# Kernel optimization log

Hardware: AMD Instinct MI355X
Metric: run time of the kernel (lower is better)

## Reference

```python
import jax, jax.numpy as jnp
import numpy as np

T = 1048576      # signal length
K = 3            # number of IMFs
ALPHA = 2000.0   # bandwidth penalty
TAU = 1e-7       # dual ascent step
TOL = 1e-6       # convergence tolerance
N_ITER = 50      # max fixed-point iterations


def _vmd(x, omega_init):
    T_ = x.shape[0]
    t = jnp.arange(1, T_ + 1, dtype=jnp.float32) / T_
    freqs = t - 0.5 - 1.0 / T_                           # [T]
    f_hat = jnp.fft.fftshift(jnp.fft.fft(x))             # [T] complex
    u0 = jnp.zeros((K, T_), dtype=f_hat.dtype)
    lam0 = jnp.zeros((T_,), dtype=f_hat.dtype)

    def step(carry, n):
        u_prev, lam_prev, omega, done = carry
        base = (freqs[None, :] - omega[:, None]) ** 2    # [K,T]
        # mode k's denom also gets (freqs-omega[k-1])^2 and (freqs-omega[k+1])^2
        nbr = jnp.zeros_like(base).at[1:].add(base[:-1]).at[:-1].add(base[1:])
        denom = base + nbr + TAU ** 2
        u_hat = (f_hat[None, :] - lam_prev[None, :] / 2.0) / (1.0 + ALPHA * denom)
        pw = jnp.real(u_hat) ** 2 + jnp.imag(u_hat) ** 2  # |u_hat|^2, [K,T]
        omega_new = jnp.sum(freqs[None, :] * pw, axis=1) / jnp.sum(pw, axis=1)
        lam_new = lam_prev + TAU * (jnp.sum(u_hat, axis=0) - f_hat)
        # convergence check (every 10th iter), mirrors the original break
        u_diff = jnp.sum(jnp.abs(u_hat - u_prev) ** 2) / jnp.sum(jnp.abs(u_prev) ** 2)
        om_diff = jnp.sum(jnp.abs(omega_new - jnp.roll(omega_new, 1))) / K
        conv = (n % 10 == 0) & (u_diff < TOL) & (om_diff < TOL)
        # freeze state once converged (break-iteration's fresh u_hat is kept)
        u_out = jnp.where(done, u_prev, u_hat)
        lam_out = jnp.where(done, lam_prev, lam_new)
        om_out = jnp.where(done, omega, omega_new)
        return (u_out, lam_out, om_out, done | conv), None

    init = (u0, lam0, omega_init.astype(jnp.float32), jnp.array(False))
    (u_hat, _, _, _), _ = jax.lax.scan(jax.checkpoint(step), init, jnp.arange(N_ITER))
    imfs = jnp.real(jnp.fft.ifft(jnp.fft.ifftshift(u_hat, axes=-1), axis=-1))
    return imfs.astype(jnp.float32)                      # [K,T]


def setup_inputs() -> dict:
    key = jax.random.key(0)
    kx, ko = jax.random.split(key)
    x = jax.random.normal(kx, (T,), dtype=jnp.float32)
    omega_init = jax.random.uniform(ko, (K,), dtype=jnp.float32) * 0.5  # init==1
    return {"x": x, "omega_init": omega_init}


def reference(x, omega_init):
    return _vmd(x, omega_init)
```

## Files before the change

kernel.cpp:

```cpp
#include <hip/hip_runtime.h>
#include <math.h>


#define ALPHA_F 2000.0f

static __device__ __forceinline__ int lpad2(int i) { return i + (i >> 4); }
static __device__ __forceinline__ int swz(int i)  { return ((i & 7) << 7) | (i >> 3); }
static __device__ __forceinline__ int swzA(int i) { return ((i & 7) << 6) | (i >> 3); }
static __device__ __forceinline__ float frcp(float x) { return __builtin_amdgcn_rcpf(x); }

typedef float v2f __attribute__((ext_vector_type(2)));
static __device__ __forceinline__ v2f sp(float s) { v2f r; r.x = s; r.y = s; return r; }
static __device__ __forceinline__ v2f v2(float a, float b) { v2f r; r.x = a; r.y = b; return r; }
static __device__ __forceinline__ v2f pkfma(v2f a, v2f b, v2f c)
{ return __builtin_elementwise_fma(a, b, c); }
static __device__ __forceinline__ v2f cmul(v2f a, v2f w)
{
  v2f t = a * sp(w.x);
  v2f s = v2(-a.y, a.x);
  return pkfma(s, sp(w.y), t);
}
static __device__ __forceinline__ v2f cmulrr(v2f a, float wr, float wi)
{
  v2f t = a * sp(wr);
  v2f s = v2(-a.y, a.x);
  return pkfma(s, sp(wi), t);
}

#define PADN2 1088

template<int CTRL>
static __device__ __forceinline__ float dpp_addf(float v)
{
  int r = __builtin_amdgcn_update_dpp(0, __float_as_int(v), CTRL, 0xf, 0xf, true);
  return v + __int_as_float(r);
}
static __device__ __forceinline__ float wave64_sum(float v)
{
  v = dpp_addf<0x111>(v);
  v = dpp_addf<0x112>(v);
  v = dpp_addf<0x114>(v);
  v = dpp_addf<0x118>(v);
  v = dpp_addf<0x142>(v);
  v = dpp_addf<0x143>(v);
  return v;
}
static __device__ __forceinline__ float row4_sum(float v)
{
  v = dpp_addf<0x111>(v);
  v = dpp_addf<0x112>(v);
  return v;
}
static __device__ __forceinline__ float rdlane(float v, int l)
{
  return __int_as_float(__builtin_amdgcn_readlane(__float_as_int(v), l));
}

template<int SIGN>
static __device__ __forceinline__ void bfly4(v2f Y0, v2f Y1, v2f Y2, v2f Y3,
    float w1r, float w1i, float w2r, float w2i, float w3r, float w3i,
    v2f& o0, v2f& o1, v2f& o2, v2f& o3)
{
  v2f y1 = cmulrr(Y1, w1r, w1i), y2 = cmulrr(Y2, w2r, w2i),
      y3 = cmulrr(Y3, w3r, w3i);
  v2f t0 = Y0 + y2, t1 = Y0 - y2, t2 = y1 + y3, t3 = y1 - y3;
  o0 = t0 + t2; o2 = t0 - t2;
  v2f ns3 = v2(t3.y, -t3.x);
  if (SIGN < 0) { o1 = t1 + ns3; o3 = t1 - ns3; }
  else          { o1 = t1 - ns3; o3 = t1 + ns3; }
}
template<int SIGN>
static __device__ __forceinline__ void bfly4_nt(v2f X0, v2f X1, v2f X2, v2f X3,
    v2f& o0, v2f& o1, v2f& o2, v2f& o3)
{
  v2f t0 = X0 + X2, t1 = X0 - X2, t2 = X1 + X3, t3 = X1 - X3;
  o0 = t0 + t2; o2 = t0 - t2;
  v2f ns3 = v2(t3.y, -t3.x);
  if (SIGN < 0) { o1 = t1 + ns3; o3 = t1 - ns3; }
  else          { o1 = t1 - ns3; o3 = t1 + ns3; }
}

template<int SIGN>
static __device__ void fft1024p_reg(v2f X0, v2f X1, v2f X2, v2f X3,
                                    v2f* A, v2f* B)
{
  const int u = threadIdx.x;
  {
    v2f o0, o1, o2, o3;
    bfly4_nt<SIGN>(X0, X1, X2, X3, o0, o1, o2, o3);
    const int base = u << 2;
    B[lpad2(base    )] = o0; B[lpad2(base + 1)] = o1;
    B[lpad2(base + 2)] = o2; B[lpad2(base + 3)] = o3;
    __syncthreads();
  }
#pragma unroll
  for (int st = 1; st < 5; ++st) {
    v2f *in  = (st & 1) ? B : A;
    v2f *out = (st & 1) ? A : B;
    const int quarter = 1 << (2 * st);
    const int p = u & (quarter - 1);
    const int g = u >> (2 * st);

    float sw, cw;
    sincospif((float)(2 * p) * (1.0f / (float)(4 << (2 * st))), &sw, &cw);
    const float w1r = cw, w1i = (SIGN < 0) ? -sw : sw;
    const float w2r = w1r * w1r - w1i * w1i, w2i = 2.0f * w1r * w1i;
    const float w3r = w2r * w1r - w2i * w1i, w3i = w2r * w1i + w2i * w1r;

    v2f o0, o1, o2, o3;
    bfly4<SIGN>(in[lpad2(u)], in[lpad2(u + 256)],
                in[lpad2(u + 512)], in[lpad2(u + 768)],
                w1r, w1i, w2r, w2i, w3r, w3i, o0, o1, o2, o3);

    const int base = (g << (2 * st + 2)) + p;
    out[lpad2(base              )] = o0;
    out[lpad2(base +     quarter)] = o1;
    out[lpad2(base + 2 * quarter)] = o2;
    out[lpad2(base + 3 * quarter)] = o3;
    __syncthreads();
  }
}

__global__ __launch_bounds__(256) void k_fwd_passA(const float* __restrict__ x,
                                                   float2* __restrict__ ws0)
{
  __shared__ __align__(16) v2f A[PADN2], B[PADN2];
  const int p = swzA(blockIdx.x);
  const int tid = threadIdx.x;
  const int c0 = 2 * p;
  v2f X[4];
#pragma unroll
  for (int q = 0; q < 4; ++q)
    X[q] = ((const v2f*)x)[(size_t)(tid + 256 * q) * 512 + p];
  fft1024p_reg<-1>(X[0], X[1], X[2], X[3], A, B);

  float sa, ca, sb, cb, ssa, cca, ssb, ccb;
  sincospif((float)(c0 * tid) * (2.0f / 1048576.0f), &sa, &ca);
  sincospif((float)((c0 + 1) * tid) * (2.0f / 1048576.0f), &sb, &cb);
  sincospif((float)c0 * (1.0f / 2048.0f), &ssa, &cca);
  sincospif((float)(c0 + 1) * (1.0f / 2048.0f), &ssb, &ccb);
  v2f E0 = v2(ca, -sa), E1 = v2(cb, -sb);
  const v2f S0 = v2(cca, -ssa), S1 = v2(ccb, -ssb);
#pragma unroll
  for (int q = 0; q < 2; ++q) {
    int k = tid + 256 * q;
    int kk = (1024 - k) & 1023;
    v2f Z = B[lpad2(k)];
    v2f Wv = B[lpad2(kk)];
    float X0r = 0.5f * (Z.x + Wv.x), X0i = 0.5f * (Z.y - Wv.y);
    float X1r = 0.5f * (Z.y + Wv.y), X1i = 0.5f * (Wv.x - Z.x);
    v2f o01 = cmul(v2(X0r, X0i), E0);
    v2f o23 = cmul(v2(X1r, X1i), E1);
    float4 o = make_float4(o01.x, o01.y, o23.x, o23.y);
    ((float4*)ws0)[(size_t)k * 512 + p] = o;
    if (q == 0) { E0 = cmul(E0, S0); E1 = cmul(E1, S1); }
  }
  if (tid == 0) {
    v2f Z = B[lpad2(512)];
    float s0, c0f, s1, c1f;
    sincospif((float)c0 * (1.0f / 1024.0f), &s0, &c0f);
    sincospif((float)(c0 + 1) * (1.0f / 1024.0f), &s1, &c1f);
    v2f o01 = cmul(v2(Z.x, 0.0f), v2(c0f, -s0));
    v2f o23 = cmul(v2(Z.y, 0.0f), v2(c1f, -s1));
    float4 o = make_float4(o01.x, o01.y, o23.x, o23.y);
    ((float4*)ws0)[(size_t)512 * 512 + p] = o;
  }
}

__global__ __launch_bounds__(256) void k_fwd_passB(const float2* __restrict__ ws0,
                                                   float2* __restrict__ fhat,
                                                   float* __restrict__ ET)
{
  __shared__ __align__(16) v2f A[PADN2], B[PADN2];
  const int b = blockIdx.x;
  const int tid = threadIdx.x;
  v2f X[4];
#pragma unroll
  for (int q = 0; q < 4; ++q)
    X[q] = ((const v2f*)ws0)[(size_t)b * 1024 + tid + 256 * q];
  fft1024p_reg<-1>(X[0], X[1], X[2], X[3], A, B);
  const bool mir = (b >= 1) && (b <= 511);
#pragma unroll
  for (int q = 0; q < 4; ++q) {
    int k2 = tid + 256 * q;
    v2f v = B[lpad2(k2)];
    float e = v.x * v.x + v.y * v.y;
    fhat[(size_t)b * 1024 + k2] = make_float2(v.x, v.y);
    ET[(size_t)k2 * 1024 + b] = e;
    if (mir) {
      fhat[(size_t)(1024 - b) * 1024 + (1023 - k2)] = make_float2(v.x, -v.y);
      ET[(size_t)(1023 - k2) * 1024 + (1024 - b)] = e;
    }
  }
}

static __device__ __forceinline__ void lag4(float x, float& l0, float& l1,
                                            float& l2, float& l3)
{
  float m0 = x, m1 = x - (1.0f / 3.0f), m2 = x - (2.0f / 3.0f), m3 = x - 1.0f;
  l0 = -4.5f * m1 * m2 * m3;
  l1 = 13.5f * m0 * m2 * m3;
  l2 = -13.5f * m0 * m1 * m3;
  l3 =  4.5f * m0 * m1 * m2;
}

__global__ __launch_bounds__(256) void k_moments(const float* __restrict__ ET,
                                                 double* __restrict__ W)
{
  __shared__ double red[4 * 4];
  const int B = blockIdx.x;
  const int k2 = B ^ 512;
  const int tid = threadIdx.x;
  double a0 = 0, a1 = 0, a2 = 0, a3 = 0;
#pragma unroll
  for (int q = 0; q < 4; ++q) {
    int k1 = tid + 256 * q;
    float e = ET[(size_t)k2 * 1024 + k1];
    float l0, l1, l2, l3;
    lag4((float)k1 * (1.0f / 1024.0f), l0, l1, l2, l3);
    a0 += (double)(e * l0); a1 += (double)(e * l1);
    a2 += (double)(e * l2); a3 += (double)(e * l3);
  }
  const int lane = tid & 63, wv = tid >> 6;
  double pv[4] = { a0, a1, a2, a3 };
#pragma unroll
  for (int j = 0; j < 4; ++j) {
    double v = pv[j];
    for (int off = 32; off; off >>= 1) v += __shfl_down(v, off, 64);
    if (lane == 0) red[wv * 4 + j] = v;
  }
  __syncthreads();
  if (tid < 4)
    W[B * 4 + tid] = red[tid] + red[4 + tid] + red[8 + tid] + red[12 + tid];
}

__global__ __launch_bounds__(256) void k_solve(
    const double* __restrict__ W4, const float* __restrict__ omega_init,
    float* __restrict__ omegaF)
{
  __shared__ float red[2][64];
  const int t = threadIdx.x;
  const int lane = t & 63, wv = t >> 6;

  float Wsc[16], fsc[16];
#pragma unroll
  for (int e = 0; e < 16; ++e) {
    Wsc[e] = (float)W4[t * 16 + e];
    int bin = 4 * t + (e >> 2);
    fsc[e] = (float)((double)bin / 1024.0 + (double)(e & 3) / 3072.0 - 0.5);
  }
  v2f frA[8], WrA[8], WfA[8];
#pragma unroll
  for (int i = 0; i < 8; ++i) {
    frA[i] = v2(fsc[2 * i], fsc[2 * i + 1]);
    WrA[i] = v2(Wsc[2 * i], Wsc[2 * i + 1]);
    WfA[i] = WrA[i] * frA[i];
  }
  float om0 = omega_init[0], om1 = omega_init[1], om2 = omega_init[2];

#pragma unroll 1
  for (int it = 0; it < 49; ++it) {
    float* rb = red[it & 1];
    v2f p0 = sp(0.f), p1 = sp(0.f), p2 = sp(0.f),
        p3 = sp(0.f), p4 = sp(0.f), p5 = sp(0.f);

#pragma unroll
    for (int i = 0; i < 8; ++i) {
      const v2f fv = frA[i];
      v2f a0 = fv - sp(om0), a1 = fv - sp(om1), a2 = fv - sp(om2);
      v2f t0 = sp(ALPHA_F) * a0, t1 = sp(ALPHA_F) * a1, t2 = sp(ALPHA_F) * a2;
      v2f m1 = pkfma(t1, a1, sp(1.0f));
      v2f dA = pkfma(t0, a0, m1);
      v2f dC = pkfma(t2, a2, m1);
      v2f dB = pkfma(t2, a2, dA);
      v2f AB = dA * dB, BC = dB * dC, AC = dA * dC;
      v2f ABC = AB * dC;
      float rr = frcp(ABC.x * ABC.y);
      v2f r = v2(rr * ABC.y, rr * ABC.x);
      v2f v0 = r * BC, v1 = r * AC, v2_ = r * AB;
      v2f g0 = v0 * v0, g1 = v1 * v1, g2 = v2_ * v2_;
      p0 = pkfma(WfA[i], g0, p0); p1 = pkfma(WfA[i], g1, p1);
      p2 = pkfma(WfA[i], g2, p2);
      p3 = pkfma(WrA[i], g0, p3); p4 = pkfma(WrA[i], g1, p4);
      p5 = pkfma(WrA[i], g2, p5);
    }

    float q0 = p0.x + p0.y, q1 = p1.x + p1.y, q2 = p2.x + p2.y;
    float q3 = p3.x + p3.y, q4 = p4.x + p4.y, q5 = p5.x + p5.y;

    q0 = wave64_sum(q0); q1 = wave64_sum(q1); q2 = wave64_sum(q2);
    q3 = wave64_sum(q3); q4 = wave64_sum(q4); q5 = wave64_sum(q5);
    if (lane == 63) {
      rb[0 * 4 + wv] = q0; rb[1 * 4 + wv] = q1; rb[2 * 4 + wv] = q2;
      rb[3 * 4 + wv] = q3; rb[4 * 4 + wv] = q4; rb[5 * 4 + wv] = q5;
    }
    __syncthreads();
    float v1r = red[it & 1][lane];
    v1r = row4_sum(v1r);
    float n0 = rdlane(v1r, 3),  n1 = rdlane(v1r, 7),  n2 = rdlane(v1r, 11);
    float e0 = rdlane(v1r, 15), e1 = rdlane(v1r, 19), e2 = rdlane(v1r, 23);
    float ie01 = frcp(e0 * e1);
    om0 = n0 * (ie01 * e1);
    om1 = n1 * (ie01 * e0);
    om2 = n2 * frcp(e2);
  }

  if (t == 0) { omegaF[0] = om0; omegaF[1] = om1; omegaF[2] = om2; }
}

__global__ __launch_bounds__(256) void k_inv_A2(
    const float2* __restrict__ fhat, const float* __restrict__ omegaF,
    float2* __restrict__ ws0)
{
  __shared__ __align__(16) v2f A[PADN2], B[PADN2];
  const int tid = threadIdx.x;
  const int bb = blockIdx.x;
  const bool pl1 = (bb >= 1024);
  const int b = pl1 ? ((bb == 1536) ? 512 : swzA(bb - 1024)) : swz(bb);
  const float om0 = omegaF[0], om1 = omegaF[1], om2 = omegaF[2];

  v2f X[4];
#pragma unroll
  for (int q = 0; q < 4; ++q) {
    int j = tid + 256 * q;
    float2 f = fhat[(size_t)b * 1024 + j];
    int bin = j ^ 512;
    int tt = (bin << 10) | b;
    float freq = (float)tt * (1.0f / 1048576.0f) - 0.5f;
    v2f fpm = v2(freq, -freq);
    v2f A0 = fpm - sp(om0), A1v = fpm - sp(om1), A2v = fpm - sp(om2);
    v2f D0 = A0 * A0, D1 = A1v * A1v, D2 = A2v * A2v;
    if (!pl1) {
      v2f DA = pkfma(sp(ALPHA_F), D0 + D1, sp(1.0f));
      v2f DB = pkfma(sp(ALPHA_F), D2, DA);
      float rrA = frcp(DA.x * DA.y);
      float rrB = frcp(DB.x * DB.y);
      float Rr = 0.5f * (rrA * DA.y + rrA * DA.x);
      float Ri = 0.5f * (rrB * DB.y + rrB * DB.x);
      X[q] = cmul(v2(f.x, f.y), v2(Rr, Ri));
    } else {
      v2f DC = pkfma(sp(ALPHA_F), D1 + D2, sp(1.0f));
      float rrC = frcp(DC.x * DC.y);
      float Rr2 = 0.5f * (rrC * DC.y + rrC * DC.x);
      X[q] = v2(f.x, f.y) * sp(Rr2);
    }
  }
  fft1024p_reg<1>(X[0], X[1], X[2], X[3], A, B);

  float sa, ca, ss, cs;
  sincospif((float)(b * tid) * (2.0f / 1048576.0f), &sa, &ca);
  sincospif((float)b * (1.0f / 2048.0f), &ss, &cs);
  v2f E = v2(ca, sa);
  const v2f S = v2(cs, ss);

  if (!pl1) {
#pragma unroll
    for (int q = 0; q < 4; ++q) {
      int m1i = tid + 256 * q;
      v2f va = B[lpad2(m1i)];
      v2f oa = cmul(va, E);
      ws0[(size_t)m1i * 1024 + b] = make_float2(oa.x, oa.y);
      E = cmul(E, S);
    }
  } else {
    const bool mir = (b >= 1) && (b <= 511);
#pragma unroll
    for (int q = 0; q < 4; ++q) {
      int m1i = tid + 256 * q;
      v2f vb = B[lpad2(m1i)];
      v2f ob = cmul(vb, E);
      ws0[1048576 + (size_t)m1i * 1024 + b] = make_float2(ob.x, ob.y);
      if (mir)
        ws0[1048576 + (size_t)m1i * 1024 + (1024 - b)] = make_float2(ob.x, -ob.y);
      E = cmul(E, S);
    }
  }
}

__global__ __launch_bounds__(256) void k_inv_B2(const float2* __restrict__ ws0,
                                                float* __restrict__ out)
{
  __shared__ __align__(16) v2f A[PADN2], B[PADN2];
  const int tid = threadIdx.x;
  const float sc = 1.0f / 1048576.0f;

  if (blockIdx.x < 1024) {
    const int b = swz(blockIdx.x);
    v2f X[4];
#pragma unroll
    for (int q = 0; q < 4; ++q)
      X[q] = ((const v2f*)ws0)[(size_t)b * 1024 + tid + 256 * q];
    fft1024p_reg<1>(X[0], X[1], X[2], X[3], A, B);
#pragma unroll
    for (int q = 0; q < 4; ++q) {
      int m2 = tid + 256 * q;
      v2f v = B[lpad2(m2)];
      out[(size_t)m2 * 1024 + b]           = v.x * sc;
      out[1048576 + (size_t)m2 * 1024 + b] = v.y * sc;
    }
  } else {
    const int s = swzA(blockIdx.x - 1024);
    const int b0 = 2 * s, b1 = 2 * s + 1;
#pragma unroll
    for (int q = 0; q < 4; ++q) {
      int j = tid + 256 * q;
      A[lpad2(j)] = ((const v2f*)ws0)[1048576 + (size_t)b0 * 1024 + j];
      B[lpad2(j)] = ((const v2f*)ws0)[1048576 + (size_t)b1 * 1024 + j];
    }
    __syncthreads();
    v2f Z[4];
#pragma unroll
    for (int q = 0; q < 4; ++q) {
      int j = tid + 256 * q;
      int mj = (1024 - j) & 1023;
      v2f W0j = A[lpad2(j)], W0m = A[lpad2(mj)];
      v2f W1j = B[lpad2(j)], W1m = B[lpad2(mj)];
      float H0r = 0.5f * (W0j.x + W0m.x), H0i = 0.5f * (W0j.y - W0m.y);
      float H1r = 0.5f * (W1j.x + W1m.x), H1i = 0.5f * (W1j.y - W1m.y);
      Z[q] = v2(H0r - H1i, H0i + H1r);
    }
    __syncthreads();
    fft1024p_reg<1>(Z[0], Z[1], Z[2], Z[3], A, B);
#pragma unroll
    for (int q = 0; q < 4; ++q) {
      int m2 = tid + 256 * q;
      v2f v = B[lpad2(m2)];
      out[2097152 + (size_t)m2 * 1024 + b0] = v.x * sc;
      out[2097152 + (size_t)m2 * 1024 + b1] = v.y * sc;
    }
  }
}

extern "C" void kernel_launch(void* const* d_in, const int* in_sizes, int n_in,
                              void* d_out, int out_size, void* d_ws, size_t ws_size,
                              hipStream_t stream)
{
  (void)in_sizes; (void)n_in; (void)out_size; (void)ws_size;
  const float* x       = (const float*)d_in[0];
  const float* om_init = (const float*)d_in[1];
  float* out = (float*)d_out;

  char* w = (char*)d_ws;
  const size_t MB = 1024ull * 1024ull;
  float2* fhat     = (float2*)(w);
  float*  ET       = (float*)(w + 8 * MB);
  double* W4       = (double*)(w + 12 * MB);
  float*  omegaF   = (float*)(w + 12 * MB + 48 * 1024);
  float2* scratch  = (float2*)(w + 16 * MB);

  k_fwd_passA<<<512, 256, 0, stream>>>(x, scratch);
  k_fwd_passB<<<513, 256, 0, stream>>>(scratch, fhat, ET);
  k_moments<<<1024, 256, 0, stream>>>(ET, W4);
  k_solve<<<1, 256, 0, stream>>>(W4, om_init, omegaF);
  k_inv_A2<<<1537, 256, 0, stream>>>(fhat, omegaF, scratch);
  k_inv_B2<<<1536, 256, 0, stream>>>(scratch, out);
}
```

Before: 161.5 us.

## Replace inverse FFT reconstruction with truncated time-domain convolution kernels

Instead of storing the full spectrum and running a two-pass inverse FFT per mode, the code builds three short real symmetric impulse responses (128 lags) from the Wiener-style filters at the solved omegas. It then convolves x directly in the time domain. This removes the fhat writes and both inverse FFT kernels, trading them for a small kernel-build pass with atomics and a cheap shared-memory convolution. It relies on the Lorentzian filter's impulse response decaying fast enough for a 128-lag truncation to stay within tolerance.

```diff
diff --git a/kernel.cpp b/kernel.cpp
--- a/kernel.cpp
+++ b/kernel.cpp
@@ -3,9 +3,9 @@
 
 
 #define ALPHA_F 2000.0f
+#define LAGS 128
 
 static __device__ __forceinline__ int lpad2(int i) { return i + (i >> 4); }
-static __device__ __forceinline__ int swz(int i)  { return ((i & 7) << 7) | (i >> 3); }
 static __device__ __forceinline__ int swzA(int i) { return ((i & 7) << 6) | (i >> 3); }
 static __device__ __forceinline__ float frcp(float x) { return __builtin_amdgcn_rcpf(x); }
 
@@ -168,7 +168,6 @@
 }
 
 __global__ __launch_bounds__(256) void k_fwd_passB(const float2* __restrict__ ws0,
-                                                   float2* __restrict__ fhat,
                                                    float* __restrict__ ET)
 {
   __shared__ __align__(16) v2f A[PADN2], B[PADN2];
@@ -185,12 +184,9 @@
     int k2 = tid + 256 * q;
     v2f v = B[lpad2(k2)];
     float e = v.x * v.x + v.y * v.y;
-    fhat[(size_t)b * 1024 + k2] = make_float2(v.x, v.y);
     ET[(size_t)k2 * 1024 + b] = e;
-    if (mir) {
-      fhat[(size_t)(1024 - b) * 1024 + (1023 - k2)] = make_float2(v.x, -v.y);
+    if (mir)
       ET[(size_t)(1023 - k2) * 1024 + (1024 - b)] = e;
-    }
   }
 }
 
@@ -236,7 +232,7 @@
 
 __global__ __launch_bounds__(256) void k_solve(
     const double* __restrict__ W4, const float* __restrict__ omega_init,
-    float* __restrict__ omegaF)
+    float* __restrict__ omegaF, float* __restrict__ kerf)
 {
   __shared__ float red[2][64];
   const int t = threadIdx.x;
@@ -305,129 +301,111 @@
     om2 = n2 * frcp(e2);
   }
 
+  for (int i = t; i < 384; i += 256) kerf[i] = 0.0f;
   if (t == 0) { omegaF[0] = om0; omegaF[1] = om1; omegaF[2] = om2; }
 }
 
-__global__ __launch_bounds__(256) void k_inv_A2(
-    const float2* __restrict__ fhat, const float* __restrict__ omegaF,
-    float2* __restrict__ ws0)
-{
-  __shared__ __align__(16) v2f A[PADN2], B[PADN2];
+__global__ __launch_bounds__(256) void k_kerbuild(const float* __restrict__ omegaF,
+                                                  float* __restrict__ kerf)
+{
+  __shared__ __align__(16) float Rs[3][2048];
   const int tid = threadIdx.x;
-  const int bb = blockIdx.x;
-  const bool pl1 = (bb >= 1024);
-  const int b = pl1 ? ((bb == 1536) ? 512 : swzA(bb - 1024)) : swz(bb);
+  const int b = blockIdx.x;
   const float om0 = omegaF[0], om1 = omegaF[1], om2 = omegaF[2];
-
-  v2f X[4];
-#pragma unroll
-  for (int q = 0; q < 4; ++q) {
-    int j = tid + 256 * q;
-    float2 f = fhat[(size_t)b * 1024 + j];
-    int bin = j ^ 512;
-    int tt = (bin << 10) | b;
-    float freq = (float)tt * (1.0f / 1048576.0f) - 0.5f;
-    v2f fpm = v2(freq, -freq);
-    v2f A0 = fpm - sp(om0), A1v = fpm - sp(om1), A2v = fpm - sp(om2);
-    v2f D0 = A0 * A0, D1 = A1v * A1v, D2 = A2v * A2v;
-    if (!pl1) {
-      v2f DA = pkfma(sp(ALPHA_F), D0 + D1, sp(1.0f));
-      v2f DB = pkfma(sp(ALPHA_F), D2, DA);
-      float rrA = frcp(DA.x * DA.y);
-      float rrB = frcp(DB.x * DB.y);
-      float Rr = 0.5f * (rrA * DA.y + rrA * DA.x);
-      float Ri = 0.5f * (rrB * DB.y + rrB * DB.x);
-      X[q] = cmul(v2(f.x, f.y), v2(Rr, Ri));
-    } else {
-      v2f DC = pkfma(sp(ALPHA_F), D1 + D2, sp(1.0f));
-      float rrC = frcp(DC.x * DC.y);
-      float Rr2 = 0.5f * (rrC * DC.y + rrC * DC.x);
-      X[q] = v2(f.x, f.y) * sp(Rr2);
+  const int f0 = b * 2048;
+#pragma unroll
+  for (int q = 0; q < 8; ++q) {
+    int idx = q * 256 + tid;
+    int fi = f0 + idx;
+    float nu = (float)(fi - 524288) * (1.0f / 1048576.0f);
+    float a0 = nu - om0, a1 = nu - om1, a2 = nu - om2;
+    float d0 = a0 * a0, d1 = a1 * a1, d2 = a2 * a2;
+    float tA = fmaf(ALPHA_F, d0 + d1, 1.0f);
+    float tB = fmaf(ALPHA_F, d2, tA);
+    float tC = fmaf(ALPHA_F, d1 + d2, 1.0f);
+    Rs[0][idx] = frcp(tA);
+    Rs[1][idx] = frcp(tB);
+    Rs[2][idx] = frcp(tC);
+  }
+  __syncthreads();
+  const int s = tid;
+  if (s >= LAGS) return;
+  float ws_, wc_;
+  sincospif((float)(4 * s) * (1.0f / 1048576.0f), &ws_, &wc_);
+  v2f acc0 = sp(0.f), acc1 = sp(0.f), acc2 = sp(0.f);
+#pragma unroll 1
+  for (int quar = 0; quar < 4; ++quar) {
+    int ubase = quar * 512;
+    v2f cr, ci;
+    {
+      float cv[2], sv[2];
+#pragma unroll
+      for (int l = 0; l < 2; ++l) {
+        int fi = f0 + ubase + l;
+        int m = (2 * s * fi) & 2097151;
+        float arg = (float)m * (1.0f / 1048576.0f);
+        float sv_, cv_;
+        sincospif(arg, &sv_, &cv_);
+        if (s & 1) { sv_ = -sv_; cv_ = -cv_; }
+        cv[l] = cv_; sv[l] = sv_;
+      }
+      cr = v2(cv[0], cv[1]); ci = v2(sv[0], sv[1]);
     }
-  }
-  fft1024p_reg<1>(X[0], X[1], X[2], X[3], A, B);
-
-  float sa, ca, ss, cs;
-  sincospif((float)(b * tid) * (2.0f / 1048576.0f), &sa, &ca);
-  sincospif((float)b * (1.0f / 2048.0f), &ss, &cs);
-  v2f E = v2(ca, sa);
-  const v2f S = v2(cs, ss);
-
-  if (!pl1) {
-#pragma unroll
-    for (int q = 0; q < 4; ++q) {
-      int m1i = tid + 256 * q;
-      v2f va = B[lpad2(m1i)];
-      v2f oa = cmul(va, E);
-      ws0[(size_t)m1i * 1024 + b] = make_float2(oa.x, oa.y);
-      E = cmul(E, S);
+#pragma unroll 4
+    for (int it = 0; it < 256; ++it) {
+      int u = ubase + 2 * it;
+      v2f r0 = *(const v2f*)&Rs[0][u];
+      v2f r1 = *(const v2f*)&Rs[1][u];
+      v2f r2 = *(const v2f*)&Rs[2][u];
+      acc0 = pkfma(r0, cr, acc0);
+      acc1 = pkfma(r1, cr, acc1);
+      acc2 = pkfma(r2, cr, acc2);
+      v2f ncr = pkfma(ci, sp(-ws_), cr * sp(wc_));
+      v2f nci = pkfma(cr, sp(ws_), ci * sp(wc_));
+      cr = ncr; ci = nci;
     }
-  } else {
-    const bool mir = (b >= 1) && (b <= 511);
-#pragma unroll
-    for (int q = 0; q < 4; ++q) {
-      int m1i = tid + 256 * q;
-      v2f vb = B[lpad2(m1i)];
-      v2f ob = cmul(vb, E);
-      ws0[1048576 + (size_t)m1i * 1024 + b] = make_float2(ob.x, ob.y);
-      if (mir)
-        ws0[1048576 + (size_t)m1i * 1024 + (1024 - b)] = make_float2(ob.x, -ob.y);
-      E = cmul(E, S);
+  }
+  const float sc = 1.0f / 1048576.0f;
+  atomicAdd(&kerf[s],       (acc0.x + acc0.y) * sc);
+  atomicAdd(&kerf[128 + s], (acc1.x + acc1.y) * sc);
+  atomicAdd(&kerf[256 + s], (acc2.x + acc2.y) * sc);
+}
+
+__global__ __launch_bounds__(256) void k_conv(const float* __restrict__ x,
+                                              const float* __restrict__ kerf,
+                                              float* __restrict__ out)
+{
+  __shared__ float xs[766];
+  __shared__ __align__(8) float kp01[2 * LAGS];
+  __shared__ float kp2[LAGS];
+  const int tid = threadIdx.x;
+  const int B = blockIdx.x;
+  const int base = B * 512 - 127;
+  for (int i = tid; i < 766; i += 256)
+    xs[i] = x[(base + i) & 1048575];
+  if (tid < LAGS) {
+    kp01[2 * tid]     = kerf[tid];
+    kp01[2 * tid + 1] = kerf[128 + tid];
+    kp2[tid]          = kerf[256 + tid];
+  }
+  __syncthreads();
+#pragma unroll
+  for (int r = 0; r < 2; ++r) {
+    int tl = r * 256 + tid;
+    int off = 127 + tl;
+    float xc = xs[off];
+    v2f a01 = (*(const v2f*)&kp01[0]) * sp(xc);
+    float a2 = kp2[0] * xc;
+#pragma unroll 4
+    for (int s = 1; s < LAGS; ++s) {
+      float pa = xs[off - s] + xs[off + s];
+      a01 = pkfma(*(const v2f*)&kp01[2 * s], sp(pa), a01);
+      a2 = fmaf(kp2[s], pa, a2);
     }
-  }
-}
-
-__global__ __launch_bounds__(256) void k_inv_B2(const float2* __restrict__ ws0,
-                                                float* __restrict__ out)
-{
-  __shared__ __align__(16) v2f A[PADN2], B[PADN2];
-  const int tid = threadIdx.x;
-  const float sc = 1.0f / 1048576.0f;
-
-  if (blockIdx.x < 1024) {
-    const int b = swz(blockIdx.x);
-    v2f X[4];
-#pragma unroll
-    for (int q = 0; q < 4; ++q)
-      X[q] = ((const v2f*)ws0)[(size_t)b * 1024 + tid + 256 * q];
-    fft1024p_reg<1>(X[0], X[1], X[2], X[3], A, B);
-#pragma unroll
-    for (int q = 0; q < 4; ++q) {
-      int m2 = tid + 256 * q;
-      v2f v = B[lpad2(m2)];
-      out[(size_t)m2 * 1024 + b]           = v.x * sc;
-      out[1048576 + (size_t)m2 * 1024 + b] = v.y * sc;
-    }
-  } else {
-    const int s = swzA(blockIdx.x - 1024);
-    const int b0 = 2 * s, b1 = 2 * s + 1;
-#pragma unroll
-    for (int q = 0; q < 4; ++q) {
-      int j = tid + 256 * q;
-      A[lpad2(j)] = ((const v2f*)ws0)[1048576 + (size_t)b0 * 1024 + j];
-      B[lpad2(j)] = ((const v2f*)ws0)[1048576 + (size_t)b1 * 1024 + j];
-    }
-    __syncthreads();
-    v2f Z[4];
-#pragma unroll
-    for (int q = 0; q < 4; ++q) {
-      int j = tid + 256 * q;
-      int mj = (1024 - j) & 1023;
-      v2f W0j = A[lpad2(j)], W0m = A[lpad2(mj)];
-      v2f W1j = B[lpad2(j)], W1m = B[lpad2(mj)];
-      float H0r = 0.5f * (W0j.x + W0m.x), H0i = 0.5f * (W0j.y - W0m.y);
-      float H1r = 0.5f * (W1j.x + W1m.x), H1i = 0.5f * (W1j.y - W1m.y);
-      Z[q] = v2(H0r - H1i, H0i + H1r);
-    }
-    __syncthreads();
-    fft1024p_reg<1>(Z[0], Z[1], Z[2], Z[3], A, B);
-#pragma unroll
-    for (int q = 0; q < 4; ++q) {
-      int m2 = tid + 256 * q;
-      v2f v = B[lpad2(m2)];
-      out[2097152 + (size_t)m2 * 1024 + b0] = v.x * sc;
-      out[2097152 + (size_t)m2 * 1024 + b1] = v.y * sc;
-    }
+    int t = B * 512 + tl;
+    out[t]           = a01.x;
+    out[1048576 + t] = a01.y;
+    out[2097152 + t] = a2;
   }
 }
 
@@ -442,16 +420,16 @@
 
   char* w = (char*)d_ws;
   const size_t MB = 1024ull * 1024ull;
-  float2* fhat     = (float2*)(w);
   float*  ET       = (float*)(w + 8 * MB);
   double* W4       = (double*)(w + 12 * MB);
   float*  omegaF   = (float*)(w + 12 * MB + 48 * 1024);
+  float*  kerf     = (float*)(w + 12 * MB + 64 * 1024);
   float2* scratch  = (float2*)(w + 16 * MB);
 
   k_fwd_passA<<<512, 256, 0, stream>>>(x, scratch);
-  k_fwd_passB<<<513, 256, 0, stream>>>(scratch, fhat, ET);
+  k_fwd_passB<<<513, 256, 0, stream>>>(scratch, ET);
   k_moments<<<1024, 256, 0, stream>>>(ET, W4);
-  k_solve<<<1, 256, 0, stream>>>(W4, om_init, omegaF);
-  k_inv_A2<<<1537, 256, 0, stream>>>(fhat, omegaF, scratch);
-  k_inv_B2<<<1536, 256, 0, stream>>>(scratch, out);
-}
+  k_solve<<<1, 256, 0, stream>>>(W4, om_init, omegaF, kerf);
+  k_kerbuild<<<512, 256, 0, stream>>>(omegaF, kerf);
+  k_conv<<<2048, 256, 0, stream>>>(x, kerf, out);
+}
```

Result: slower. 203.2 us (+25.8%).
